# Kernel optimization log

Measured on AMD Instinct MI355X. Metric: run time of the kernel, lower is better.

The kernel has to match this reference:

```python
import jax, jax.numpy as jnp
import numpy as np

GROUP = 16  # FP4 quantization group size along the K (channel) axis
FP4_MAX = 6.0  # max magnitude representable in e2m1


def _round_e2m1(v):
    """Round to nearest value on the signed e2m1 grid {0,.5,1,1.5,2,3,4,6}."""
    s = jnp.sign(v)
    a = jnp.clip(jnp.abs(v), 0.0, FP4_MAX)
    q = jnp.where(a < 0.25, 0.0,
        jnp.where(a < 0.75, 0.5,
        jnp.where(a < 1.25, 1.0,
        jnp.where(a < 1.75, 1.5,
        jnp.where(a < 2.5, 2.0,
        jnp.where(a < 3.5, 3.0,
        jnp.where(a < 5.0, 4.0, 6.0)))))))
    return s * q


def fake_quant_fp4(x):
    """NVFP4-style fake quantization: per-16 group fp8_e4m3 scale + e2m1 values.

    x: [..., K] with K % 16 == 0. Returns dequantized tensor, same shape/dtype.
    """
    shp = x.shape
    g = x.reshape(shp[:-1] + (shp[-1] // GROUP, GROUP))
    amax = jnp.max(jnp.abs(g), axis=-1, keepdims=True)
    # scale stored as fp8_e4m3 (matches oscales dtype float8_e4m3fn in source)
    scale = (amax / FP4_MAX).astype(jnp.float8_e4m3fn).astype(x.dtype)
    safe = jnp.where(scale > 0, scale, jnp.ones_like(scale))
    q = _round_e2m1(g / safe)
    dq = jnp.where(scale > 0, q * scale, jnp.zeros_like(q))
    return dq.reshape(shp)


def setup_inputs() -> dict:
    key = jax.random.key(0)
    k1, k2, k3 = jax.random.split(key, 3)
    M, K, N = 8192, 4096, 4096
    x = jax.random.normal(k1, (M, K), dtype=jnp.float32)
    weight = jax.random.normal(k2, (N, K), dtype=jnp.float32) * 0.02
    bias = jax.random.normal(k3, (N,), dtype=jnp.float32) * 0.01
    return {"x": x, "weight": weight, "bias": bias}


def reference(x, weight, bias):
    # quantize_input: per-group FP4 fake-quant of activations (smooth == ones)
    xq = fake_quant_fp4(x)
    # __init__ quantizes weight_pad with the same kernel -> qweight/wscales
    wq = fake_quant_fp4(weight)
    # gemm_w4a4 with inline dequant + bias add
    out = jnp.einsum("mk,nk->mn", xq, wq) + bias
    return out
```

## Files before the change

### kernel.cpp

```cpp
#include <hip/hip_runtime.h>
#include <cstdint>


typedef __attribute__((ext_vector_type(8))) __bf16 bf16x8;
typedef __attribute__((ext_vector_type(4))) float f32x4;

typedef __attribute__((address_space(1))) void gvoid;
typedef __attribute__((address_space(3))) void lvoid;

__device__ __forceinline__ float fp8_e4m3_rt(float x) {
    if (x < 0.015625f) {
        return __builtin_rintf(x * 512.0f) * (1.0f / 512.0f);
    }
    unsigned u = __float_as_uint(x);
    unsigned lsb = (u >> 20) & 1u;
    u = (u + 0x7FFFFu + lsb) & ~0xFFFFFu;
    return __uint_as_float(u);
}

__device__ __forceinline__ float round_e2m1(float v) {
    float a = fabsf(v);
    a = fminf(a, 6.0f);
    float q = a < 0.25f ? 0.0f :
              a < 0.75f ? 0.5f :
              a < 1.25f ? 1.0f :
              a < 1.75f ? 1.5f :
              a < 2.5f  ? 2.0f :
              a < 3.5f  ? 3.0f :
              a < 5.0f  ? 4.0f : 6.0f;
    return copysignf(q, v);
}

__global__ __launch_bounds__(256) void quant_fp4(const float* __restrict__ in,
                                                 uint16_t* __restrict__ out,
                                                 int nquads) {
    int i = blockIdx.x * 256 + threadIdx.x;
    if (i >= nquads) return;
    float4 v = ((const float4*)in)[i];
    float a = fmaxf(fmaxf(fabsf(v.x), fabsf(v.y)), fmaxf(fabsf(v.z), fabsf(v.w)));
    a = fmaxf(a, __shfl_xor(a, 1));
    a = fmaxf(a, __shfl_xor(a, 2));
    float scale = fp8_e4m3_rt(a / 6.0f);
    float safe = scale > 0.0f ? scale : 1.0f;
    float vals[4] = {v.x, v.y, v.z, v.w};
    unsigned r[4];
    #pragma unroll
    for (int e = 0; e < 4; ++e) {
        float q = round_e2m1(vals[e] / safe);
        float dq = scale > 0.0f ? q * scale : 0.0f;
        r[e] = __float_as_uint(dq) >> 16;
    }
    uint2 o;
    o.x = r[0] | (r[1] << 16);
    o.y = r[2] | (r[3] << 16);
    ((uint2*)out)[i] = o;
}

#define BM 128
#define BN 128
#define BK 32

__global__ __launch_bounds__(256)
void gemm_w4a4(const uint16_t* __restrict__ Aq, const uint16_t* __restrict__ Bq,
               const float* __restrict__ bias, float* __restrict__ C,
               int M, int N, int K) {
    __shared__ __align__(16) uint16_t lA[BM * BK];
    __shared__ __align__(16) uint16_t lB[BN * BK];

    const int t    = threadIdx.x;
    const int wave = t >> 6;
    const int lane = t & 63;
    const int wm   = (wave >> 1) * 64;
    const int wn   = (wave & 1) * 64;
    const int mBase = blockIdx.y * BM;
    const int nBase = blockIdx.x * BN;
    const int lrow = lane & 15;
    const int kq   = (lane >> 4) * 8;

    f32x4 acc[4][4] = {};

    for (int k0 = 0; k0 < K; k0 += BK) {
        #pragma unroll
        for (int it = 0; it < 2; ++it) {
            const int c   = it * 256 + t;
            const int row = c >> 2;
            const int kc  = (c & 3) * 8;
            const uint16_t* gA = Aq + (size_t)(mBase + row) * K + (k0 + kc);
            const uint16_t* gB = Bq + (size_t)(nBase + row) * K + (k0 + kc);
            const int ldsOff = (it * 256 + wave * 64) * 8;
            __builtin_amdgcn_global_load_lds((gvoid*)gA, (lvoid*)&lA[ldsOff], 16, 0, 0);
            __builtin_amdgcn_global_load_lds((gvoid*)gB, (lvoid*)&lB[ldsOff], 16, 0, 0);
        }
        __syncthreads();

        bf16x8 af[4], bfr[4];
        #pragma unroll
        for (int i = 0; i < 4; ++i)
            af[i] = *(const bf16x8*)&lA[(wm + i * 16 + lrow) * BK + kq];
        #pragma unroll
        for (int j = 0; j < 4; ++j)
            bfr[j] = *(const bf16x8*)&lB[(wn + j * 16 + lrow) * BK + kq];

        #pragma unroll
        for (int i = 0; i < 4; ++i)
            #pragma unroll
            for (int j = 0; j < 4; ++j)
                acc[i][j] = __builtin_amdgcn_mfma_f32_16x16x32_bf16(
                    af[i], bfr[j], acc[i][j], 0, 0, 0);
        __syncthreads();
    }

    const int rq = (lane >> 4) * 4;
    #pragma unroll
    for (int j = 0; j < 4; ++j) {
        const int col = nBase + wn + j * 16 + lrow;
        const float bj = bias[col];
        #pragma unroll
        for (int i = 0; i < 4; ++i) {
            const int row0 = mBase + wm + i * 16 + rq;
            #pragma unroll
            for (int r = 0; r < 4; ++r)
                C[(size_t)(row0 + r) * N + col] = acc[i][j][r] + bj;
        }
    }
}

extern "C" void kernel_launch(void* const* d_in, const int* in_sizes, int n_in,
                              void* d_out, int out_size, void* d_ws, size_t ws_size,
                              hipStream_t stream) {
    const float* x    = (const float*)d_in[0];
    const float* w    = (const float*)d_in[1];
    const float* bias = (const float*)d_in[2];
    float* out = (float*)d_out;

    const int N = in_sizes[2];
    const int K = in_sizes[1] / N;
    const int M = in_sizes[0] / K;

    uint16_t* xq = (uint16_t*)d_ws;
    uint16_t* wq = xq + (size_t)M * K;

    const int xquads = (M * K) / 4;
    const int wquads = (N * K) / 4;
    quant_fp4<<<(xquads + 255) / 256, 256, 0, stream>>>(x, xq, xquads);
    quant_fp4<<<(wquads + 255) / 256, 256, 0, stream>>>(w, wq, wquads);

    dim3 grid(N / BN, M / BM);
    gemm_w4a4<<<grid, 256, 0, stream>>>(xq, wq, bias, out, M, N, K);
}
```

Measured before the change: 600.2 us.

## Store LDS tiles in MFMA fragment order and fold scale into quant thresholds

```diff
diff --git a/kernel.cpp b/kernel.cpp
--- a/kernel.cpp
+++ b/kernel.cpp
@@ -18,19 +18,6 @@
     return __uint_as_float(u);
 }
 
-__device__ __forceinline__ float round_e2m1(float v) {
-    float a = fabsf(v);
-    a = fminf(a, 6.0f);
-    float q = a < 0.25f ? 0.0f :
-              a < 0.75f ? 0.5f :
-              a < 1.25f ? 1.0f :
-              a < 1.75f ? 1.5f :
-              a < 2.5f  ? 2.0f :
-              a < 3.5f  ? 3.0f :
-              a < 5.0f  ? 4.0f : 6.0f;
-    return copysignf(q, v);
-}
-
 __global__ __launch_bounds__(256) void quant_fp4(const float* __restrict__ in,
                                                  uint16_t* __restrict__ out,
                                                  int nquads) {
@@ -40,14 +27,25 @@
     float a = fmaxf(fmaxf(fabsf(v.x), fabsf(v.y)), fmaxf(fabsf(v.z), fabsf(v.w)));
     a = fmaxf(a, __shfl_xor(a, 1));
     a = fmaxf(a, __shfl_xor(a, 2));
-    float scale = fp8_e4m3_rt(a / 6.0f);
-    float safe = scale > 0.0f ? scale : 1.0f;
+    float s = fp8_e4m3_rt(a / 6.0f);
+    const float t0 = 0.25f * s, t1 = 0.75f * s, t2 = 1.25f * s, t3 = 1.75f * s,
+                t4 = 2.5f * s, t5 = 3.5f * s, t6 = 5.0f * s;
+    const float p1 = 0.5f * s, p2 = s, p3 = 1.5f * s, p4 = 2.0f * s,
+                p5 = 3.0f * s, p6 = 4.0f * s, p7 = 6.0f * s;
     float vals[4] = {v.x, v.y, v.z, v.w};
     unsigned r[4];
     #pragma unroll
     for (int e = 0; e < 4; ++e) {
-        float q = round_e2m1(vals[e] / safe);
-        float dq = scale > 0.0f ? q * scale : 0.0f;
+        float x = vals[e];
+        float ax = fabsf(x);
+        float dq = ax < t0 ? 0.0f :
+                   ax < t1 ? p1 :
+                   ax < t2 ? p2 :
+                   ax < t3 ? p3 :
+                   ax < t4 ? p4 :
+                   ax < t5 ? p5 :
+                   ax < t6 ? p6 : p7;
+        dq = copysignf(dq, x);
         r[e] = __float_as_uint(dq) >> 16;
     }
     uint2 o;
@@ -75,31 +73,31 @@
     const int mBase = blockIdx.y * BM;
     const int nBase = blockIdx.x * BN;
     const int lrow = lane & 15;
-    const int kq   = (lane >> 4) * 8;
+
+    const int sRow = lrow;
+    const int sKc  = (lane >> 4) * 8;
 
     f32x4 acc[4][4] = {};
 
     for (int k0 = 0; k0 < K; k0 += BK) {
         #pragma unroll
-        for (int it = 0; it < 2; ++it) {
-            const int c   = it * 256 + t;
-            const int row = c >> 2;
-            const int kc  = (c & 3) * 8;
-            const uint16_t* gA = Aq + (size_t)(mBase + row) * K + (k0 + kc);
-            const uint16_t* gB = Bq + (size_t)(nBase + row) * K + (k0 + kc);
-            const int ldsOff = (it * 256 + wave * 64) * 8;
-            __builtin_amdgcn_global_load_lds((gvoid*)gA, (lvoid*)&lA[ldsOff], 16, 0, 0);
-            __builtin_amdgcn_global_load_lds((gvoid*)gB, (lvoid*)&lB[ldsOff], 16, 0, 0);
+        for (int p = 0; p < 2; ++p) {
+            const int s   = wave * 2 + p;
+            const int row = s * 16 + sRow;
+            const uint16_t* gA = Aq + (size_t)(mBase + row) * K + (k0 + sKc);
+            const uint16_t* gB = Bq + (size_t)(nBase + row) * K + (k0 + sKc);
+            __builtin_amdgcn_global_load_lds((gvoid*)gA, (lvoid*)&lA[s * 512], 16, 0, 0);
+            __builtin_amdgcn_global_load_lds((gvoid*)gB, (lvoid*)&lB[s * 512], 16, 0, 0);
         }
         __syncthreads();
 
         bf16x8 af[4], bfr[4];
         #pragma unroll
         for (int i = 0; i < 4; ++i)
-            af[i] = *(const bf16x8*)&lA[(wm + i * 16 + lrow) * BK + kq];
+            af[i] = *(const bf16x8*)&lA[((wave >> 1) * 4 + i) * 512 + lane * 8];
         #pragma unroll
         for (int j = 0; j < 4; ++j)
-            bfr[j] = *(const bf16x8*)&lB[(wn + j * 16 + lrow) * BK + kq];
+            bfr[j] = *(const bf16x8*)&lB[((wave & 1) * 4 + j) * 512 + lane * 8];
 
         #pragma unroll
         for (int i = 0; i < 4; ++i)
```

Measured after the change: 776.6 us. 1.29x slower.
